# Kernel optimization log

Hardware: AMD Instinct MI355X
Metric: run time of the kernel (lower is better)

Reference implementation:

```python
import jax, jax.numpy as jnp
import numpy as np

N_HEAD = 25

def setup_inputs() -> dict:
    key = jax.random.key(0)
    k1, k2, k3 = jax.random.split(key, 3)
    B, T, C = 2, 2048, 1600
    x = jax.random.normal(k1, (B, T, C), dtype=jnp.float32)
    w_qkv = jax.random.normal(k2, (C, 3 * C), dtype=jnp.float32) * (1.0 / np.sqrt(C))
    b_qkv = jnp.zeros((3 * C,), dtype=jnp.float32)
    w_out = jax.random.normal(k3, (C, C), dtype=jnp.float32) * (1.0 / np.sqrt(C))
    b_out = jnp.zeros((C,), dtype=jnp.float32)
    return {"x": x, "w_qkv": w_qkv, "b_qkv": b_qkv, "w_out": w_out, "b_out": b_out}

def reference(x, w_qkv, b_qkv, w_out, b_out):
    B, T, C = x.shape
    H = N_HEAD
    D = C // H  # head_dim = 64
    qkv = jnp.einsum('btc,cd->btd', x, w_qkv) + b_qkv  # [B,T,3C]
    q, k, v = jnp.split(qkv, 3, axis=-1)
    # [B,T,C] -> [B,H,T,D]
    q = q.reshape(B, T, H, D).transpose(0, 2, 1, 3)
    k = k.reshape(B, T, H, D).transpose(0, 2, 1, 3)
    v = v.reshape(B, T, H, D).transpose(0, 2, 1, 3)
    scale = 1.0 / jnp.sqrt(jnp.float32(D))
    scores = jnp.einsum('bhqd,bhkd->bhqk', q, k) * scale  # [B,H,T,T]
    causal = jnp.tril(jnp.ones((T, T), dtype=bool))
    scores = jnp.where(causal, scores, jnp.float32(-1e10))
    attn = jax.nn.softmax(scores, axis=-1)
    out = jnp.einsum('bhqk,bhkd->bhqd', attn, v)  # [B,H,T,D]
    out = out.transpose(0, 2, 1, 3).reshape(B, T, C)
    return jnp.einsum('btc,cd->btd', out, w_out) + b_out
```

## Files before the change

kernel.cpp:

```cpp
#include <hip/hip_runtime.h>
#include <cstdint>
#include <cstddef>

typedef unsigned short u16;
typedef __attribute__((ext_vector_type(8))) short bhalf8;
typedef __attribute__((ext_vector_type(4))) float fx4;
typedef __attribute__((ext_vector_type(4))) unsigned short u16x4;

#define T_SEQ 2048
#define NHEAD 25
#define QKV_LD 4864
#define WOUT_LD 1664

static __device__ __forceinline__ u16 f2bf(float f) {
  union { float f; uint32_t u; } v; v.f = f;
  uint32_t r = (v.u + 0x7FFFu + ((v.u >> 16) & 1u)) >> 16;
  return (u16)r;
}

static __device__ __forceinline__ fx4 mfma16(bhalf8 a, bhalf8 b, fx4 c) {
  return __builtin_amdgcn_mfma_f32_16x16x32_bf16(a, b, c, 0, 0, 0);
}

static __device__ __forceinline__ void async16(const void* g, void* l) {
  __builtin_amdgcn_global_load_lds(
      (__attribute__((address_space(1))) unsigned int*)(void*)g,
      (__attribute__((address_space(3))) unsigned int*)l, 16, 0, 0);
}

__global__ void cvt_bf16_kernel(const float* __restrict__ in, u16* __restrict__ out, int n4) {
  int i = blockIdx.x * 256 + threadIdx.x;
  if (i >= n4) return;
  float4 v = ((const float4*)in)[i];
  u16x4 o;
  o.x = f2bf(v.x); o.y = f2bf(v.y); o.z = f2bf(v.z); o.w = f2bf(v.w);
  ((u16x4*)out)[i] = o;
}

__global__ void transp_cvt_kernel(const float* __restrict__ in, u16* __restrict__ out,
                                  int R, int C) {
  __shared__ float tile[32][33];
  int bx = blockIdx.x * 32, by = blockIdx.y * 32;
  int tx = threadIdx.x, ty = threadIdx.y;
  #pragma unroll
  for (int i = 0; i < 32; i += 8)
    tile[ty + i][tx] = in[(size_t)(by + ty + i) * C + bx + tx];
  __syncthreads();
  #pragma unroll
  for (int i = 0; i < 32; i += 8)
    out[(size_t)(bx + ty + i) * R + by + tx] = f2bf(tile[tx][ty + i]);
}

template<int BN, bool OUTF32>
__global__ __launch_bounds__(256)
void gemm_bt_kernel(const u16* __restrict__ A, const u16* __restrict__ BT,
                    const float* __restrict__ bias, void* __restrict__ C,
                    int K, int ldc, int Nreal) {
  constexpr int BM = 128, BK = 32;
  constexpr int NF = BN / 32;
  constexpr int APASS = (BM * BK) / (256 * 8);
  constexpr int BPASS = (BN * BK) / (256 * 8);
  __shared__ __align__(16) u16 Al[BM * BK];
  __shared__ __align__(16) u16 Bl[BN * BK];
  const int t = threadIdx.x;
  const int w = t >> 6, l = t & 63, lr = l & 15, lg = l >> 4;
  const int wm = w >> 1, wn = w & 1;

  const int nwg = gridDim.x * gridDim.y;
  const int id = blockIdx.y * gridDim.x + blockIdx.x;
  const int qq = nwg >> 3;
  const int swz = (id & 7) * qq + (id >> 3);
  const int bx = swz % gridDim.x, by = swz / gridDim.x;

  const int m0 = by * BM, n0 = bx * BN;

  fx4 acc[4][NF] = {};

  for (int k0 = 0; k0 < K; k0 += BK) {
    #pragma unroll
    for (int p = 0; p < APASS; ++p) {
      int c = t + p * 256;
      async16(A + (size_t)(m0 + (c >> 2)) * K + k0 + (c & 3) * 8, Al + c * 8);
    }
    #pragma unroll
    for (int p = 0; p < BPASS; ++p) {
      int c = t + p * 256;
      async16(BT + (size_t)(n0 + (c >> 2)) * K + k0 + (c & 3) * 8, Bl + c * 8);
    }
    __syncthreads();
    bhalf8 af[4], bfr[NF];
    #pragma unroll
    for (int m = 0; m < 4; ++m)
      af[m] = *(const bhalf8*)(Al + (wm * 64 + m * 16 + lr) * BK + lg * 8);
    #pragma unroll
    for (int n = 0; n < NF; ++n)
      bfr[n] = *(const bhalf8*)(Bl + (wn * (BN / 2) + n * 16 + lr) * BK + lg * 8);
    #pragma unroll
    for (int m = 0; m < 4; ++m)
      #pragma unroll
      for (int n = 0; n < NF; ++n)
        acc[m][n] = mfma16(af[m], bfr[n], acc[m][n]);
    __syncthreads();
  }

  #pragma unroll
  for (int m = 0; m < 4; ++m)
  #pragma unroll
  for (int n = 0; n < NF; ++n)
  #pragma unroll
  for (int r = 0; r < 4; ++r) {
    int gr = m0 + wm * 64 + m * 16 + lg * 4 + r;
    int gc = n0 + wn * (BN / 2) + n * 16 + lr;
    float bv = (gc < Nreal) ? bias[gc] : 0.0f;
    float v = acc[m][n][r] + bv;
    if constexpr (OUTF32) {
      if (gc < Nreal) ((float*)C)[(size_t)gr * ldc + gc] = v;
    } else {
      ((u16*)C)[(size_t)gr * ldc + gc] = f2bf(v);
    }
  }
}

#define KSWZ(row, slot) (((row) << 6) + ((((slot)) ^ ((row) & 7)) << 3))

__global__ __launch_bounds__(256, 3)
void attn_kernel(const u16* __restrict__ qkv, u16* __restrict__ out) {
  const int qblk = (gridDim.x - 1) - blockIdx.x;
  const int bh = blockIdx.y;
  const int b = bh / NHEAD, h = bh % NHEAD;
  const int t = threadIdx.x, w = t >> 6, l = t & 63;
  const int lr = l & 15, lg = l >> 4;

  __shared__ __align__(16) u16 Kl[2][64 * 64];
  __shared__ __align__(16) u16 Vt[2][64 * 64];
  __shared__ __align__(16) u16 Pl[4][32][72];

  const int q0 = qblk * 128;
  const int qw = q0 + w * 32;
  const int nkb = 2 * qblk + 2;

  bhalf8 qf[2][2];
  #pragma unroll
  for (int g = 0; g < 2; ++g) {
    const size_t qoff = ((size_t)(b * T_SEQ + qw + g * 16 + lr)) * QKV_LD + h * 64;
    qf[g][0] = *(const bhalf8*)(qkv + qoff + lg * 8);
    qf[g][1] = *(const bhalf8*)(qkv + qoff + 32 + lg * 8);
  }

  constexpr float KSC = 0.125f * 1.44269504089f;

  fx4 oacc[2][4] = {};
  float m_run[2][4], mk[2][4], thr[2][4], l_acc[2][4];
  #pragma unroll
  for (int g = 0; g < 2; ++g)
    #pragma unroll
    for (int r = 0; r < 4; ++r) {
      m_run[g][r] = -3.0e38f; mk[g][r] = -3.0e38f; thr[g][r] = -3.0e38f; l_acc[g][r] = 0.0f;
    }

  const size_t kvrow_base = (size_t)(b * T_SEQ) * QKV_LD + 1600 + h * 64;

  int4 vpre[2];
  #pragma unroll
  for (int p = 0; p < 2; ++p) {
    const int c = t + p * 256;
    const int kr = c >> 3;
    const int ks = (c & 7) ^ (kr & 7);
    const size_t rb = kvrow_base + (size_t)kr * QKV_LD;
    async16(qkv + rb + ks * 8, Kl[0] + c * 8);
    vpre[p] = *(const int4*)(qkv + rb + 1600 + (c & 7) * 8);
  }

  for (int kb = 0; kb < nkb; ++kb) {
    const int bsel = kb & 1;
    const int kv0 = kb * 64;
    u16* Klb = Kl[bsel];
    u16* Vtb = Vt[bsel];

    asm volatile("s_waitcnt vmcnt(0)" ::: "memory");
    #pragma unroll
    for (int p = 0; p < 2; ++p) {
      const int c = t + p * 256;
      const int vr = c >> 3;
      const int vc = (c & 7) * 8;
      union { int4 v; u16 u[8]; } vv; vv.v = vpre[p];
      #pragma unroll
      for (int i = 0; i < 8; ++i) {
        int row = vc + i;
        Vtb[(row << 6) + (((vr >> 3) ^ (row & 7)) << 3) + (vr & 7)] = vv.u[i];
      }
    }
    __syncthreads();

    if (kb + 1 < nkb) {
      #pragma unroll
      for (int p = 0; p < 2; ++p) {
        const int c = t + p * 256;
        const int kr = c >> 3;
        const int ks = (c & 7) ^ (kr & 7);
        const size_t rb = kvrow_base + (size_t)(kv0 + 64 + kr) * QKV_LD;
        async16(qkv + rb + ks * 8, Kl[bsel ^ 1] + c * 8);
        vpre[p] = *(const int4*)(qkv + rb + 1600 + (c & 7) * 8);
      }
    }

    const bool active = (kv0 <= qw + 31);
    if (active) {
      float sv[2][4][4];
      __builtin_amdgcn_s_setprio(1);
      #pragma unroll
      for (int n = 0; n < 4; ++n) {
        bhalf8 k0f = *(const bhalf8*)(Klb + KSWZ(n * 16 + lr, lg));
        bhalf8 k1f = *(const bhalf8*)(Klb + KSWZ(n * 16 + lr, 4 + lg));
        #pragma unroll
        for (int g = 0; g < 2; ++g) {
          fx4 s = {0.f, 0.f, 0.f, 0.f};
          s = mfma16(qf[g][0], k0f, s);
          s = mfma16(qf[g][1], k1f, s);
          #pragma unroll
          for (int r = 0; r < 4; ++r) sv[g][n][r] = s[r];
        }
      }
      __builtin_amdgcn_s_setprio(0);
      if (kv0 + 63 > qw) {
        #pragma unroll
        for (int g = 0; g < 2; ++g)
          #pragma unroll
          for (int n = 0; n < 4; ++n)
            #pragma unroll
            for (int r = 0; r < 4; ++r)
              if (kv0 + n * 16 + lr > qw + g * 16 + lg * 4 + r) sv[g][n][r] = -1e30f;
      }
      float pm[2][4];
      bool ok = true;
      #pragma unroll
      for (int g = 0; g < 2; ++g)
        #pragma unroll
        for (int r = 0; r < 4; ++r) {
          pm[g][r] = fmaxf(fmaxf(sv[g][0][r], sv[g][1][r]), fmaxf(sv[g][2][r], sv[g][3][r]));
          ok = ok && (pm[g][r] <= thr[g][r]);
        }
      if (!__all(ok)) {
        #pragma unroll
        for (int g = 0; g < 2; ++g)
          #pragma unroll
          for (int r = 0; r < 4; ++r) {
            float mx = pm[g][r] * 0.125f;
            mx = fmaxf(mx, __shfl_xor(mx, 1));
            mx = fmaxf(mx, __shfl_xor(mx, 2));
            mx = fmaxf(mx, __shfl_xor(mx, 4));
            mx = fmaxf(mx, __shfl_xor(mx, 8));
            float mN = fmaxf(m_run[g][r], mx);
            float scl = __expf(m_run[g][r] - mN);
            m_run[g][r] = mN;
            mk[g][r] = mN * 1.44269504089f;
            thr[g][r] = 8.0f * mN + 64.0f;
            l_acc[g][r] *= scl;
            oacc[g][0][r] *= scl; oacc[g][1][r] *= scl;
            oacc[g][2][r] *= scl; oacc[g][3][r] *= scl;
          }
      }
      #pragma unroll
      for (int g = 0; g < 2; ++g)
        #pragma unroll
        for (int n = 0; n < 4; ++n)
          #pragma unroll
          for (int r = 0; r < 4; ++r) {
            float p = exp2f(fmaf(sv[g][n][r], KSC, -mk[g][r]));
            l_acc[g][r] += p;
            Pl[w][g * 16 + lg * 4 + r][n * 16 + lr] = f2bf(p);
          }
      asm volatile("s_waitcnt lgkmcnt(0)" ::: "memory");
      __builtin_amdgcn_sched_barrier(0);
      __builtin_amdgcn_s_setprio(1);
      #pragma unroll
      for (int s = 0; s < 2; ++s) {
        bhalf8 pa0 = *(const bhalf8*)&Pl[w][lr][s * 32 + lg * 8];
        bhalf8 pa1 = *(const bhalf8*)&Pl[w][16 + lr][s * 32 + lg * 8];
        #pragma unroll
        for (int n = 0; n < 4; ++n) {
          bhalf8 vbf = *(const bhalf8*)(Vtb + KSWZ(n * 16 + lr, s * 4 + lg));
          oacc[0][n] = mfma16(pa0, vbf, oacc[0][n]);
          oacc[1][n] = mfma16(pa1, vbf, oacc[1][n]);
        }
      }
      __builtin_amdgcn_s_setprio(0);
    }
  }

  #pragma unroll
  for (int g = 0; g < 2; ++g) {
    #pragma unroll
    for (int r = 0; r < 4; ++r) {
      float rs = l_acc[g][r];
      rs += __shfl_xor(rs, 1);
      rs += __shfl_xor(rs, 2);
      rs += __shfl_xor(rs, 4);
      rs += __shfl_xor(rs, 8);
      l_acc[g][r] = rs;
    }
    const size_t obase = ((size_t)(b * T_SEQ + qw + g * 16 + lg * 4)) * 1600 + h * 64;
    #pragma unroll
    for (int n = 0; n < 4; ++n)
      #pragma unroll
      for (int r = 0; r < 4; ++r) {
        float v = oacc[g][n][r] / l_acc[g][r];
        out[obase + (size_t)r * 1600 + n * 16 + lr] = f2bf(v);
      }
  }
}

extern "C" void kernel_launch(void* const* d_in, const int* in_sizes, int n_in,
                              void* d_out, int out_size, void* d_ws, size_t ws_size,
                              hipStream_t stream) {
  const float* x     = (const float*)d_in[0];
  const float* w_qkv = (const float*)d_in[1];
  const float* b_qkv = (const float*)d_in[2];
  const float* w_out = (const float*)d_in[3];
  const float* b_out = (const float*)d_in[4];
  float* out = (float*)d_out;

  constexpr size_t NTOK = 4096;
  char* ws = (char*)d_ws;
  size_t off = 0;
  u16* xb    = (u16*)(ws + off); off += NTOK * 1600 * 2;
  u16* wqkvT = (u16*)(ws + off); off += (size_t)QKV_LD * 1600 * 2;
  u16* woutT = (u16*)(ws + off); off += (size_t)WOUT_LD * 1600 * 2;
  u16* qkvb  = (u16*)(ws + off); off += NTOK * QKV_LD * 2;
  u16* attnb = (u16*)(ws + off); off += NTOK * 1600 * 2;
  (void)ws_size; (void)in_sizes; (void)n_in; (void)out_size;

  cvt_bf16_kernel<<<dim3((unsigned)(NTOK * 1600 / 4 / 256)), dim3(256), 0, stream>>>(
      x, xb, (int)(NTOK * 1600 / 4));
  transp_cvt_kernel<<<dim3(4800 / 32, 1600 / 32), dim3(32, 8), 0, stream>>>(
      w_qkv, wqkvT, 1600, 4800);
  transp_cvt_kernel<<<dim3(1600 / 32, 1600 / 32), dim3(32, 8), 0, stream>>>(
      w_out, woutT, 1600, 1600);
  gemm_bt_kernel<128, false><<<dim3(QKV_LD / 128, NTOK / 128), dim3(256), 0, stream>>>(
      xb, wqkvT, b_qkv, qkvb, 1600, QKV_LD, 4800);
  attn_kernel<<<dim3(T_SEQ / 128, 2 * NHEAD), dim3(256), 0, stream>>>(qkvb, attnb);
  gemm_bt_kernel<128, true><<<dim3(WOUT_LD / 128, NTOK / 128), dim3(256), 0, stream>>>(
      attnb, woutT, b_out, out, 1600, 1600, 1600);
}
```

Before: 446.4 us.

## Split long causal query blocks across two KV chunks with a merge kernel

Query blocks 8-15 of the attention now process their key range in two 1024-key chunks on separate workgroups. Each chunk writes unnormalized fp32 partial outputs plus row max and sum, and a new merge kernel combines them into the bf16 attention output. The grid goes from 16 to 24 slots per head, ordered to balance the causal work per workgroup and shorten the tail. The cost is the extra partial-output traffic and one more kernel launch.

Measured after the change: 380.6 us. 1.17x faster.

```diff
diff --git a/kernel.cpp b/kernel.cpp
--- a/kernel.cpp
+++ b/kernel.cpp
@@ -123,9 +123,16 @@
 
 #define KSWZ(row, slot) (((row) << 6) + ((((slot)) ^ ((row) & 7)) << 3))
 
+__device__ const unsigned char SLOT_Q[24] =
+    {8,9,10,11,12,13,14,15,15,7,14,6,13,5,12,4,11,3,10,2,9,1,8,0};
+__device__ const unsigned char SLOT_C[24] =
+    {0,0,0,0,0,0,0,0, 1,0, 1,0, 1,0, 1,0, 1,0, 1,0, 1,0, 1,0};
+
 __global__ __launch_bounds__(256, 3)
-void attn_kernel(const u16* __restrict__ qkv, u16* __restrict__ out) {
-  const int qblk = (gridDim.x - 1) - blockIdx.x;
+void attn_kernel(const u16* __restrict__ qkv, u16* __restrict__ out,
+                 float* __restrict__ Opart, float2* __restrict__ MLpart) {
+  const int slot = blockIdx.x;
+  const int qblk = SLOT_Q[slot], chunk = SLOT_C[slot];
   const int bh = blockIdx.y;
   const int b = bh / NHEAD, h = bh % NHEAD;
   const int t = threadIdx.x, w = t >> 6, l = t & 63;
@@ -137,7 +144,8 @@
 
   const int q0 = qblk * 128;
   const int qw = q0 + w * 32;
-  const int nkb = 2 * qblk + 2;
+  const int kv_begin = chunk << 10;
+  const int kv_end = min((qblk + 1) << 7, kv_begin + 1024);
 
   bhalf8 qf[2][2];
   #pragma unroll
@@ -166,14 +174,13 @@
     const int c = t + p * 256;
     const int kr = c >> 3;
     const int ks = (c & 7) ^ (kr & 7);
-    const size_t rb = kvrow_base + (size_t)kr * QKV_LD;
+    const size_t rb = kvrow_base + (size_t)(kv_begin + kr) * QKV_LD;
     async16(qkv + rb + ks * 8, Kl[0] + c * 8);
     vpre[p] = *(const int4*)(qkv + rb + 1600 + (c & 7) * 8);
   }
 
-  for (int kb = 0; kb < nkb; ++kb) {
-    const int bsel = kb & 1;
-    const int kv0 = kb * 64;
+  for (int kv0 = kv_begin; kv0 < kv_end; kv0 += 64) {
+    const int bsel = ((kv0 - kv_begin) >> 6) & 1;
     u16* Klb = Kl[bsel];
     u16* Vtb = Vt[bsel];
 
@@ -192,7 +199,7 @@
     }
     __syncthreads();
 
-    if (kb + 1 < nkb) {
+    if (kv0 + 64 < kv_end) {
       #pragma unroll
       for (int p = 0; p < 2; ++p) {
         const int c = t + p * 256;
@@ -289,7 +296,7 @@
   }
 
   #pragma unroll
-  for (int g = 0; g < 2; ++g) {
+  for (int g = 0; g < 2; ++g)
     #pragma unroll
     for (int r = 0; r < 4; ++r) {
       float rs = l_acc[g][r];
@@ -299,15 +306,62 @@
       rs += __shfl_xor(rs, 8);
       l_acc[g][r] = rs;
     }
-    const size_t obase = ((size_t)(b * T_SEQ + qw + g * 16 + lg * 4)) * 1600 + h * 64;
-    #pragma unroll
-    for (int n = 0; n < 4; ++n)
-      #pragma unroll
-      for (int r = 0; r < 4; ++r) {
-        float v = oacc[g][n][r] / l_acc[g][r];
-        out[obase + (size_t)r * 1600 + n * 16 + lr] = f2bf(v);
-      }
-  }
+
+  if (qblk < 8) {
+    #pragma unroll
+    for (int g = 0; g < 2; ++g) {
+      const size_t obase = ((size_t)(b * T_SEQ + qw + g * 16 + lg * 4)) * 1600 + h * 64;
+      #pragma unroll
+      for (int n = 0; n < 4; ++n)
+        #pragma unroll
+        for (int r = 0; r < 4; ++r) {
+          float v = oacc[g][n][r] / l_acc[g][r];
+          out[obase + (size_t)r * 1600 + n * 16 + lr] = f2bf(v);
+        }
+    }
+  } else {
+    const int pslot = ((qblk - 8) << 1) | chunk;
+    const int prow0 = (bh * 16 + pslot) * 128 + w * 32;
+    #pragma unroll
+    for (int g = 0; g < 2; ++g) {
+      #pragma unroll
+      for (int n = 0; n < 4; ++n)
+        #pragma unroll
+        for (int r = 0; r < 4; ++r)
+          Opart[(size_t)(prow0 + g * 16 + lg * 4 + r) * 64 + n * 16 + lr] = oacc[g][n][r];
+      if (lr == 0) {
+        #pragma unroll
+        for (int r = 0; r < 4; ++r)
+          MLpart[prow0 + g * 16 + lg * 4 + r] = make_float2(l_acc[g][r], mk[g][r]);
+      }
+    }
+  }
+}
+
+__global__ __launch_bounds__(256)
+void merge_kernel(const float* __restrict__ Opart, const float2* __restrict__ MLpart,
+                  u16* __restrict__ out) {
+  const int e = blockIdx.x * 256 + threadIdx.x;
+  const int d4 = (e & 15) << 2;
+  const int row1024 = (e >> 4) & 1023;
+  const int bh = e >> 14;
+  const int b = bh / NHEAD, h = bh % NHEAD;
+  const int qblk8 = row1024 >> 7;
+  const int base0 = (bh * 16 + (qblk8 << 1)) * 128 + (row1024 & 127);
+  const int base1 = base0 + 128;
+
+  float2 ml0 = MLpart[base0], ml1 = MLpart[base1];
+  float M = fmaxf(ml0.y, ml1.y);
+  float w0 = exp2f(ml0.y - M), w1 = exp2f(ml1.y - M);
+  float linv = 1.0f / (w0 * ml0.x + w1 * ml1.x);
+  float4 o0 = *(const float4*)(Opart + (size_t)base0 * 64 + d4);
+  float4 o1 = *(const float4*)(Opart + (size_t)base1 * 64 + d4);
+  u16x4 ov;
+  ov.x = f2bf((w0 * o0.x + w1 * o1.x) * linv);
+  ov.y = f2bf((w0 * o0.y + w1 * o1.y) * linv);
+  ov.z = f2bf((w0 * o0.z + w1 * o1.z) * linv);
+  ov.w = f2bf((w0 * o0.w + w1 * o1.w) * linv);
+  *(u16x4*)(out + ((size_t)(b * T_SEQ + 1024 + row1024)) * 1600 + h * 64 + d4) = ov;
 }
 
 extern "C" void kernel_launch(void* const* d_in, const int* in_sizes, int n_in,
@@ -328,6 +382,8 @@
   u16* woutT = (u16*)(ws + off); off += (size_t)WOUT_LD * 1600 * 2;
   u16* qkvb  = (u16*)(ws + off); off += NTOK * QKV_LD * 2;
   u16* attnb = (u16*)(ws + off); off += NTOK * 1600 * 2;
+  float*  Opart  = (float*)(ws + off);  off += (size_t)50 * 16 * 128 * 64 * 4;
+  float2* MLpart = (float2*)(ws + off); off += (size_t)50 * 16 * 128 * 8;
   (void)ws_size; (void)in_sizes; (void)n_in; (void)out_size;
 
   cvt_bf16_kernel<<<dim3((unsigned)(NTOK * 1600 / 4 / 256)), dim3(256), 0, stream>>>(
@@ -338,7 +394,8 @@
       w_out, woutT, 1600, 1600);
   gemm_bt_kernel<128, false><<<dim3(QKV_LD / 128, NTOK / 128), dim3(256), 0, stream>>>(
       xb, wqkvT, b_qkv, qkvb, 1600, QKV_LD, 4800);
-  attn_kernel<<<dim3(T_SEQ / 128, 2 * NHEAD), dim3(256), 0, stream>>>(qkvb, attnb);
+  attn_kernel<<<dim3(24, 2 * NHEAD), dim3(256), 0, stream>>>(qkvb, attnb, Opart, MLpart);
+  merge_kernel<<<dim3(50 * 1024 * 16 / 256), dim3(256), 0, stream>>>(Opart, MLpart, attnb);
   gemm_bt_kernel<128, true><<<dim3(WOUT_LD / 128, NTOK / 128), dim3(256), 0, stream>>>(
       attnb, woutT, b_out, out, 1600, 1600, 1600);
 }
```
